# Performance work log

Hardware: AMD Instinct MI355X
Metric: run time of the kernel (lower is better)

Reference implementation:

```python
import jax, jax.numpy as jnp
import numpy as np

DIM = 512
HEADS = 8
DH = 64
INNER = HEADS * DH  # 512
GRID = 32
FH, FW = GRID, GRID // 2 + 1


def _group_norm1(x, g, b, eps=1e-5):
    # GroupNorm(1, C) on NHWC: normalize over (H, W, C) per sample, per-channel affine
    mu = jnp.mean(x, axis=(1, 2, 3), keepdims=True)
    var = jnp.var(x, axis=(1, 2, 3), keepdims=True)
    return (x - mu) * jax.lax.rsqrt(var + eps) * g + b


def setup_inputs() -> dict:
    key = jax.random.key(0)
    ks = jax.random.split(key, 12)
    B, N, C = 8, GRID * GRID + 1, DIM
    s = 0.02
    return {
        "x": jax.random.normal(ks[0], (B, N, C), jnp.float32),
        "Wq": jax.random.normal(ks[1], (C, INNER), jnp.float32) * s,
        "Wk": jax.random.normal(ks[2], (C, INNER), jnp.float32) * s,
        "Wv": jax.random.normal(ks[3], (C, INNER), jnp.float32) * s,
        "dw_w": jax.random.normal(ks[4], (3, 3, 1, C), jnp.float32) * s,   # depthwise, HWIO
        "pw_w": jax.random.normal(ks[5], (C, INNER), jnp.float32) * s,     # 1x1 conv
        "ln_g": jnp.ones((INNER,), jnp.float32),
        "ln_b": jnp.zeros((INNER,), jnp.float32),
        "fr_wr": jnp.ones((FH, FW, C), jnp.float32),    # learnable FFT filter (real)
        "fr_wi": jnp.zeros((FH, FW, C), jnp.float32),   # learnable FFT filter (imag)
        "fr_pw": jax.random.normal(ks[6], (C, INNER), jnp.float32) * s,
        "fr_g": jnp.ones((INNER,), jnp.float32),
        "fr_b": jnp.zeros((INNER,), jnp.float32),
        "g_W1": jax.random.normal(ks[7], (3 * INNER, 3 * INNER // 4), jnp.float32) * s,
        "g_b1": jnp.zeros((3 * INNER // 4,), jnp.float32),
        "g_W2": jax.random.normal(ks[8], (3 * INNER // 4, 3), jnp.float32) * s,
        "g_b2": jnp.zeros((3,), jnp.float32),
        "Wp": jax.random.normal(ks[9], (INNER, DIM), jnp.float32) * s,
        "bp": jnp.zeros((DIM,), jnp.float32),
        "h_feat": GRID,
        "w_feat": GRID,
    }


def reference(x, Wq, Wk, Wv, dw_w, pw_w, ln_g, ln_b, fr_wr, fr_wi, fr_pw, fr_g, fr_b,
              g_W1, g_b1, g_W2, g_b2, Wp, bp, h_feat, w_feat):
    B, N, C = x.shape
    scale = DH ** -0.5
    has_cls = (N == h_feat * w_feat + 1)
    spatial = x[:, 1:] if has_cls else x

    # Branch 1: global self-attention (manual softmax attention)
    q = (x @ Wq).reshape(B, N, HEADS, DH)
    k = (x @ Wk).reshape(B, N, HEADS, DH)
    v = (x @ Wv).reshape(B, N, HEADS, DH)
    attn = jax.nn.softmax(jnp.einsum('bihd,bjhd->bhij', q, k) * scale, axis=-1)
    glob = jnp.einsum('bhij,bjhd->bihd', attn, v).reshape(B, N, INNER)

    # Branch 2: local depthwise conv -> pointwise conv -> GroupNorm(1)
    sp = spatial.reshape(B, h_feat, w_feat, C)  # NHWC
    dw = jax.lax.conv_general_dilated(sp, dw_w, (1, 1), 'SAME',
                                      dimension_numbers=('NHWC', 'HWIO', 'NHWC'),
                                      feature_group_count=C)
    loc = _group_norm1(jnp.einsum('bhwc,co->bhwo', dw, pw_w), ln_g, ln_b)
    loc = loc.reshape(B, h_feat * w_feat, INNER)
    if has_cls:
        loc = jnp.concatenate([loc.mean(axis=1, keepdims=True), loc], axis=1)

    # Branch 3: frequency enhancement (rfft2 -> learnable complex filter -> irfft2)
    xf = jnp.fft.rfft2(sp, axes=(1, 2), norm='ortho')               # (B, FH, FW, C)
    xf = xf * jax.lax.complex(fr_wr, fr_wi)[None]
    xe = jnp.fft.irfft2(xf, s=(h_feat, w_feat), axes=(1, 2), norm='ortho')
    fr = jax.nn.gelu(_group_norm1(jnp.einsum('bhwc,co->bhwo', xe, fr_pw), fr_g, fr_b),
                     approximate=False)
    fr = fr.reshape(B, h_feat * w_feat, INNER)
    if has_cls:
        fr = jnp.concatenate([fr.mean(axis=1, keepdims=True), fr], axis=1)

    # Gate MLP + softmax fusion
    cat = jnp.concatenate([glob, loc, fr], axis=-1)                  # (B, N, 3*INNER)
    gw = jax.nn.softmax(jax.nn.gelu(cat @ g_W1 + g_b1, approximate=False) @ g_W2 + g_b2,
                        axis=-1)                                     # (B, N, 3)
    fused = gw[..., 0:1] * glob + gw[..., 1:2] * loc + gw[..., 2:3] * fr
    return fused @ Wp + bp
```

## Files before the change

kernel.cpp:

```cpp
#include <hip/hip_runtime.h>
#include <math.h>

#define BB 8
#define NT 1025
#define CD 512
#define NH 8
#define DHD 64
#define HW 1024
#define FWD 17
#define MTOK 8200
#define MPAD 8320
#define QKS 1536

typedef __attribute__((ext_vector_type(8))) short short8;
typedef __attribute__((ext_vector_type(4))) float f32x4;
typedef __attribute__((ext_vector_type(16))) float f32x16;
typedef __attribute__((ext_vector_type(4))) unsigned u32x4;

__device__ __forceinline__ float gelu_exact(float x){
  return 0.5f * x * (1.0f + erff(x * 0.70710678118654752f));
}

__device__ __forceinline__ short f2bf(float f){
  unsigned u = __float_as_uint(f);
  unsigned r = (u + 0x7FFFu + ((u >> 16) & 1u)) >> 16;
  return (short)r;
}

__device__ __forceinline__ float bf2f(short s){
  unsigned u = ((unsigned)(unsigned short)s) << 16;
  return __uint_as_float(u);
}

__device__ __forceinline__ unsigned cvt_pk_bf16(float lo, float hi){
  unsigned r;
  asm volatile("v_cvt_pk_bf16_f32 %0, %1, %2" : "=v"(r) : "v"(lo), "v"(hi));
  return r;
}

__device__ __forceinline__ int xcd_logical(int phys, int n){
  int xcd = phys & 7, slot = phys >> 3;
  int q = n >> 3, r = n & 7;
  return xcd*q + (xcd < r ? xcd : r) + slot;
}

__global__ __launch_bounds__(256) void wconv_all(
    const float* __restrict__ Wq, const float* __restrict__ Wk, const float* __restrict__ Wv,
    const float* __restrict__ pw, const float* __restrict__ frpw,
    const float* __restrict__ gW1, const float* __restrict__ Wp,
    short* __restrict__ wqkvt, short* __restrict__ pwt, short* __restrict__ frpwt,
    short* __restrict__ gw1t, short* __restrict__ wpt)
{
  const int t = blockIdx.x;
  const float* W; short* Wt; int K, N, idx; float scale = 1.0f;
  if      (t < 256) { W = Wq;   Wt = wqkvt;            K=512;  N=512; idx=t;       scale=0.125f; }
  else if (t < 512) { W = Wk;   Wt = wqkvt+512*512;    K=512;  N=512; idx=t-256; }
  else if (t < 768) { W = Wv;   Wt = wqkvt+1024*512;   K=512;  N=512; idx=t-512; }
  else if (t < 1024){ W = pw;   Wt = pwt;              K=512;  N=512; idx=t-768; }
  else if (t < 1280){ W = frpw; Wt = frpwt;            K=512;  N=512; idx=t-1024; }
  else if (t < 1856){ W = gW1;  Wt = gw1t;             K=1536; N=384; idx=t-1280; }
  else              { W = Wp;   Wt = wpt;              K=512;  N=512; idx=t-1856; }
  const int ntn = N >> 5;
  const int n0 = (idx % ntn) << 5, k0 = (idx / ntn) << 5;
  __shared__ float tl[32][33];
  const int tx = threadIdx.x & 31, ty = threadIdx.x >> 5;
  #pragma unroll
  for (int i = 0; i < 32; i += 8)
    tl[ty+i][tx] = W[(size_t)(k0+ty+i)*N + n0+tx];
  __syncthreads();
  #pragma unroll
  for (int i = 0; i < 32; i += 8)
    Wt[(size_t)(n0+ty+i)*K + k0+tx] = f2bf(tl[tx][ty+i] * scale);
}

__global__ __launch_bounds__(256) void x2bf(const float* __restrict__ x, short* __restrict__ xb)
{
  size_t i = ((size_t)blockIdx.x*256 + threadIdx.x) * 8;
  if (i >= (size_t)MPAD*CD) return;
  size_t row = i >> 9;
  short8 o;
  if (row < MTOK){
    #pragma unroll
    for (int j = 0; j < 8; j++) o[j] = f2bf(x[i+j]);
  } else {
    #pragma unroll
    for (int j = 0; j < 8; j++) o[j] = 0;
  }
  *(short8*)(xb + i) = o;
}


#define GEMM_DECL                                                          \
  __shared__ short As[2][128*64];                                          \
  __shared__ short Bs[2][64*64];                                           \
  const int tid = threadIdx.x;                                             \
  const int lane = tid & 63, wv = tid >> 6;                                \
  const int lc = lane & 15, lg = lane >> 4;                                \
  short8 ra[4], rb[2];                                                     \
  f32x4 acc[2][4];                                                         \
  _Pragma("unroll")                                                        \
  for (int rt=0;rt<2;rt++)                                                 \
    _Pragma("unroll")                                                      \
    for (int ct=0;ct<4;ct++) acc[rt][ct] = (f32x4){0.f,0.f,0.f,0.f};

#define GEMM_LOADA(Aptr, Kst, k0)                                          \
  _Pragma("unroll")                                                        \
  for (int p = 0; p < 4; p++){                                             \
    int c = tid + p*256; int r = c >> 3, s = c & 7;                        \
    ra[p] = *(const short8*)((Aptr) + (size_t)(row0 + r)*(Kst) + (k0) + s*8); \
  }

#define GEMM_LOADB(Bptr, Kst, k0)                                          \
  _Pragma("unroll")                                                        \
  for (int p = 0; p < 2; p++){                                             \
    int c = tid + p*256; int r = c >> 3, s = c & 7;                        \
    rb[p] = *(const short8*)((Bptr) + (size_t)(col0 + r)*(Kst) + (k0) + s*8); \
  }

#define GEMM_WRITES(buf)                                                   \
  _Pragma("unroll")                                                        \
  for (int p = 0; p < 4; p++){                                             \
    int c = tid + p*256; int r = c >> 3, s = c & 7;                        \
    *(short8*)&As[buf][r*64 + ((s ^ (r & 7))*8)] = ra[p];                  \
  }                                                                        \
  _Pragma("unroll")                                                        \
  for (int p = 0; p < 2; p++){                                             \
    int c = tid + p*256; int r = c >> 3, s = c & 7;                        \
    *(short8*)&Bs[buf][r*64 + ((s ^ (r & 7))*8)] = rb[p];                  \
  }

#define GEMM_COMPUTE(buf)                                                  \
  _Pragma("unroll")                                                        \
  for (int ks = 0; ks < 2; ks++){                                          \
    short8 af[2], bfr[4];                                                  \
    _Pragma("unroll")                                                      \
    for (int rt = 0; rt < 2; rt++){                                        \
      int r = wv*32 + rt*16 + lc;                                          \
      af[rt] = *(const short8*)&As[buf][r*64 + (((ks*4+lg) ^ (r & 7))*8)]; \
    }                                                                      \
    _Pragma("unroll")                                                      \
    for (int ct = 0; ct < 4; ct++){                                        \
      int r = ct*16 + lc;                                                  \
      bfr[ct] = *(const short8*)&Bs[buf][r*64 + (((ks*4+lg) ^ (r & 7))*8)];\
    }                                                                      \
    _Pragma("unroll")                                                      \
    for (int rt = 0; rt < 2; rt++)                                         \
      _Pragma("unroll")                                                    \
      for (int ct = 0; ct < 4; ct++)                                       \
        acc[rt][ct] = __builtin_amdgcn_mfma_f32_16x16x32_bf16(af[rt], bfr[ct], acc[rt][ct], 0,0,0); \
  }

__global__ __launch_bounds__(256) void gemm_bf16(
    const short* __restrict__ A, const short* __restrict__ Bt,
    const float* __restrict__ bias, void* __restrict__ Cm,
    int M, int N, int K, int flags)
{
  const int l = xcd_logical(blockIdx.x, gridDim.x);
  const int nx = N >> 6;
  const int row0 = (l / nx) * 128, col0 = (l % nx) * 64;
  GEMM_DECL;

  const int nk = K >> 6;
  GEMM_LOADA(A, K, 0); GEMM_LOADB(Bt, K, 0);
  GEMM_WRITES(0);
  __syncthreads();
  for (int kt = 0; kt < nk; kt++){
    const int cur = kt & 1;
    if (kt + 1 < nk){ GEMM_LOADA(A, K, (kt+1)*64); GEMM_LOADB(Bt, K, (kt+1)*64); }
    GEMM_COMPUTE(cur);
    if (kt + 1 < nk){
      GEMM_WRITES(cur ^ 1);
      __syncthreads();
    }
  }

  #pragma unroll
  for (int rt = 0; rt < 2; rt++)
    #pragma unroll
    for (int e = 0; e < 4; e++){
      int gr = row0 + wv*32 + rt*16 + lg*4 + e;
      if (gr >= M) continue;
      #pragma unroll
      for (int ct = 0; ct < 4; ct++){
        int gc = col0 + ct*16 + lc;
        float v = acc[rt][ct][e];
        if (flags & 1) v += bias[gc];
        if (flags & 2) v = gelu_exact(v);
        if (flags & 4) ((short*)Cm)[(size_t)gr*N + gc] = f2bf(v);
        else           ((float*)Cm)[(size_t)gr*N + gc] = v;
      }
    }
}

__global__ __launch_bounds__(256) void gemm_pw2(
    const short* __restrict__ A0, const short* __restrict__ B0,
    const short* __restrict__ A1, const short* __restrict__ B1,
    short* __restrict__ C0, short* __restrict__ C1,
    float* __restrict__ totL, float* __restrict__ totF)
{
  const int l = xcd_logical(blockIdx.x, 1024);
  const int bx = l & 7;
  const int by = (l >> 3) & 63;
  const int br = l >> 9;
  const short* A  = br ? A1 : A0;
  const short* Bt = br ? B1 : B0;
  short* Cm       = br ? C1 : C0;
  float* tot      = br ? totF : totL;
  const int N = 512, K = 512;
  const int row0 = by * 128, col0 = bx * 64;
  GEMM_DECL;

  const int nk = 8;
  GEMM_LOADA(A, K, 0); GEMM_LOADB(Bt, K, 0);
  GEMM_WRITES(0);
  __syncthreads();
  for (int kt = 0; kt < nk; kt++){
    const int cur = kt & 1;
    if (kt + 1 < nk){ GEMM_LOADA(A, K, (kt+1)*64); GEMM_LOADB(Bt, K, (kt+1)*64); }
    GEMM_COMPUTE(cur);
    if (kt + 1 < nk){
      GEMM_WRITES(cur ^ 1);
      __syncthreads();
    }
  }

  float s1 = 0.f, s2 = 0.f;
  #pragma unroll
  for (int rt = 0; rt < 2; rt++)
    #pragma unroll
    for (int e = 0; e < 4; e++){
      int gr = row0 + wv*32 + rt*16 + lg*4 + e;
      #pragma unroll
      for (int ct = 0; ct < 4; ct++){
        int gc = col0 + ct*16 + lc;
        float v = acc[rt][ct][e];
        Cm[(size_t)gr*N + gc] = f2bf(v);
        s1 += v; s2 += v*v;
      }
    }
  #pragma unroll
  for (int o = 32; o > 0; o >>= 1){ s1 += __shfl_xor(s1, o); s2 += __shfl_xor(s2, o); }
  if (lane == 0){
    atomicAdd(&tot[(row0>>10)*2],   s1);
    atomicAdd(&tot[(row0>>10)*2+1], s2);
  }
}

__global__ __launch_bounds__(256) void gemm_gate(
    const short* __restrict__ A0, const short* __restrict__ A1, const short* __restrict__ A2,
    const short* __restrict__ Bt, const float* __restrict__ bias, short* __restrict__ Cm,
    int M)
{
  const int N = 384, K = 1536;
  const int l = xcd_logical(blockIdx.x, gridDim.x);
  const int row0 = (l / 6) * 128, col0 = (l % 6) * 64;
  GEMM_DECL;

  const int nk = 24;
  auto loadAg = [&](int kt2){
    int k0 = kt2 * 64;
    const short* Asrc = (k0 < 512) ? A0 : (k0 < 1024 ? A1 : A2);
    const int kb = k0 & 511;
    GEMM_LOADA(Asrc, 512, kb);
  };
  loadAg(0); GEMM_LOADB(Bt, K, 0);
  GEMM_WRITES(0);
  __syncthreads();
  for (int kt = 0; kt < nk; kt++){
    const int cur = kt & 1;
    if (kt + 1 < nk){ loadAg(kt+1); GEMM_LOADB(Bt, K, (kt+1)*64); }
    GEMM_COMPUTE(cur);
    if (kt + 1 < nk){
      GEMM_WRITES(cur ^ 1);
      __syncthreads();
    }
  }

  #pragma unroll
  for (int rt = 0; rt < 2; rt++)
    #pragma unroll
    for (int e = 0; e < 4; e++){
      int gr = row0 + wv*32 + rt*16 + lg*4 + e;
      if (gr >= M) continue;
      #pragma unroll
      for (int ct = 0; ct < 4; ct++){
        int gc = col0 + ct*16 + lc;
        float v = acc[rt][ct][e] + bias[gc];
        Cm[(size_t)gr*N + gc] = f2bf(gelu_exact(v));
      }
    }
}

__global__ __launch_bounds__(256) void attn_mfma32(
    const short* __restrict__ qkv, short* __restrict__ glob)
{
  const int bi = blockIdx.x;
  const int xcd = bi & 7;
  const int jj = bi >> 3;
  const int gq = jj / 9;
  const int qt = jj - gq*9;
  const int g  = xcd + 8*gq;
  const int h  = g & 7, b = g >> 3;

  const int tid = threadIdx.x;
  const int lane = tid & 63, wq = tid >> 6;
  const int q32 = lane & 31;
  const int hi  = lane >> 5;
  const int bN = b * NT;
  const int q0w = qt*128 + wq*32;

  __shared__ short Kl[2][64*64];
  __shared__ short Vl[2][64*64];

  short8 qf[4];
  {
    int qr = q0w + q32; if (qr > 1024) qr = 1024;
    const short* qp = qkv + (size_t)(bN + qr)*QKS + h*DHD + hi*8;
    qf[0] = *(const short8*)(qp);
    qf[1] = *(const short8*)(qp + 16);
    qf[2] = *(const short8*)(qp + 32);
    qf[3] = *(const short8*)(qp + 48);
  }

  f32x16 oA = {0.f,0.f,0.f,0.f,0.f,0.f,0.f,0.f,0.f,0.f,0.f,0.f,0.f,0.f,0.f,0.f};
  f32x16 oB = oA;
  float rs = 0.f;

  const int kc0 = tid;
  const int kc1 = tid + 256;
  const int vkey = tid & 63, vdg = tid >> 6;
  const short* kgbase = qkv + (size_t)bN*QKS + 512 + h*DHD;
  const short* vgbase = qkv + (size_t)bN*QKS + 1024 + h*DHD;

  short8 gk0, gk1, gv0, gv1;
  auto loadT = [&](int kt2){
    gk0 = *(const short8*)(kgbase + (size_t)(kt2*64 + (kc0>>3))*QKS + (kc0&7)*8);
    gk1 = *(const short8*)(kgbase + (size_t)(kt2*64 + (kc1>>3))*QKS + (kc1&7)*8);
    gv0 = *(const short8*)(vgbase + (size_t)(kt2*64 + vkey)*QKS + vdg*16);
    gv1 = *(const short8*)(vgbase + (size_t)(kt2*64 + vkey)*QKS + vdg*16 + 8);
  };
  auto writeT = [&](int buf){
    { int r = kc0>>3, sl = kc0&7;
      *(short8*)&Kl[buf][r*64 + (((sl) ^ (r&7))*8)] = gk0; }
    { int r = kc1>>3, sl = kc1&7;
      *(short8*)&Kl[buf][r*64 + (((sl) ^ (r&7))*8)] = gk1; }
    #pragma unroll
    for (int i2 = 0; i2 < 8; i2++){
      int d0 = vdg*16 + i2, d1 = vdg*16 + 8 + i2;
      Vl[buf][d0*64 + (((vkey>>3) ^ (d0&7))*8) + (vkey&7)] = gv0[i2];
      Vl[buf][d1*64 + (((vkey>>3) ^ (d1&7))*8) + (vkey&7)] = gv1[i2];
    }
  };

  loadT(0);
  writeT(0);
  __syncthreads();

  for (int kt = 0; kt < 17; kt++){
    const int cur = kt & 1;
    if (kt < 16) loadT(kt+1);

    #pragma unroll
    for (int ks = 0; ks < 2; ks++){
      f32x16 s = {0.f,0.f,0.f,0.f,0.f,0.f,0.f,0.f,0.f,0.f,0.f,0.f,0.f,0.f,0.f,0.f};
      const int krow = ks*32 + q32;
      const int kbase = krow*64;
      const int kx = q32 & 7;
      __builtin_amdgcn_s_setprio(1);
      #pragma unroll
      for (int kk = 0; kk < 4; kk++){
        short8 af = *(const short8*)&Kl[cur][kbase + (((2*kk+hi) ^ kx)*8)];
        s = __builtin_amdgcn_mfma_f32_32x32x16_bf16(af, qf[kk], s, 0,0,0);
      }
      __builtin_amdgcn_s_setprio(0);
      float p[16];
      if (kt == 16){
        #pragma unroll
        for (int e = 0; e < 16; e++){
          bool valid = (ks == 0) && (e == 0) && (hi == 0);
          p[e] = valid ? __expf(s[e]) : 0.f;
        }
      } else {
        #pragma unroll
        for (int e = 0; e < 16; e++) p[e] = __expf(s[e]);
      }
      #pragma unroll
      for (int e = 0; e < 16; e++) rs += p[e];
      unsigned pk[4][2];
      #pragma unroll
      for (int g2 = 0; g2 < 4; g2++){
        pk[g2][0] = cvt_pk_bf16(p[4*g2+0], p[4*g2+1]);
        pk[g2][1] = cvt_pk_bf16(p[4*g2+2], p[4*g2+3]);
      }
      #pragma unroll
      for (int kc = 0; kc < 2; kc++){
        unsigned e00 = pk[2*kc][0],   e01 = pk[2*kc][1];
        unsigned e10 = pk[2*kc+1][0], e11 = pk[2*kc+1][1];
        unsigned t00 = (unsigned)__shfl_xor((int)e00, 32);
        unsigned t01 = (unsigned)__shfl_xor((int)e01, 32);
        unsigned t10 = (unsigned)__shfl_xor((int)e10, 32);
        unsigned t11 = (unsigned)__shfl_xor((int)e11, 32);
        u32x4 pu;
        pu[0] = hi ? t10 : e00;
        pu[1] = hi ? t11 : e01;
        pu[2] = hi ? e10 : t00;
        pu[3] = hi ? e11 : t01;
        short8 pa = *(short8*)&pu;
        const int vsl = 4*ks + 2*kc + hi;
        __builtin_amdgcn_s_setprio(1);
        {
          short8 vf0 = *(const short8*)&Vl[cur][(q32)*64      + ((vsl ^ kx)*8)];
          oA = __builtin_amdgcn_mfma_f32_32x32x16_bf16(pa, vf0, oA, 0,0,0);
          short8 vf1 = *(const short8*)&Vl[cur][(32+q32)*64   + ((vsl ^ kx)*8)];
          oB = __builtin_amdgcn_mfma_f32_32x32x16_bf16(pa, vf1, oB, 0,0,0);
        }
        __builtin_amdgcn_s_setprio(0);
      }
    }

    if (kt < 16){
      writeT(cur ^ 1);
      __syncthreads();
    }
  }

  float rs_tot = rs + __shfl_xor(rs, 32);
  #pragma unroll
  for (int e = 0; e < 16; e++){
    int rowr = (e & 3) + 8*(e >> 2) + 4*hi;
    int q = q0w + rowr;
    if (q > 1024) continue;
    float inv = 1.0f / __shfl(rs_tot, rowr);
    size_t base = (size_t)(bN + q)*CD + h*DHD + q32;
    glob[base]      = f2bf(oA[e] * inv);
    glob[base + 32] = f2bf(oB[e] * inv);
  }
}

__global__ __launch_bounds__(512) void dwconv(
    const short* __restrict__ xb, const float* __restrict__ w, short* __restrict__ out)
{
  const int c = threadIdx.x;
  const int xx = blockIdx.x & 31;
  const int yg = (blockIdx.x >> 5) & 7;
  const int b  = blockIdx.x >> 8;
  const int y0 = yg << 2;
  float acc[4] = {0.f,0.f,0.f,0.f};
  #pragma unroll
  for (int dx = -1; dx <= 1; dx++){
    int x2 = xx + dx;
    if (x2 < 0 || x2 > 31) continue;
    float col[6];
    #pragma unroll
    for (int r = 0; r < 6; r++){
      int row = y0 - 1 + r;
      col[r] = (row >= 0 && row < 32)
             ? bf2f(xb[((size_t)(b*NT + 1 + row*32 + x2))*CD + c]) : 0.f;
    }
    float w0 = w[(0*3+dx+1)*CD + c];
    float w1 = w[(1*3+dx+1)*CD + c];
    float w2 = w[(2*3+dx+1)*CD + c];
    #pragma unroll
    for (int o = 0; o < 4; o++)
      acc[o] += col[o]*w0 + col[o+1]*w1 + col[o+2]*w2;
  }
  #pragma unroll
  for (int o = 0; o < 4; o++)
    out[((size_t)(b*HW + (y0+o)*32 + xx))*CD + c] = f2bf(acc[o]);
}

__global__ __launch_bounds__(512) void gn_apply2(
    const short* __restrict__ mmL, const short* __restrict__ mmF,
    const float* __restrict__ totL, const float* __restrict__ totF,
    const float* __restrict__ gL, const float* __restrict__ bL,
    const float* __restrict__ gF, const float* __restrict__ bF,
    short* __restrict__ loc, short* __restrict__ fr,
    float* __restrict__ colsumL, float* __restrict__ colsumF)
{
  const int br = blockIdx.x >> 8;
  const int bi = blockIdx.x & 255;
  const int c = threadIdx.x;
  const int b = bi >> 5;
  const int p0 = (bi & 31) << 5;
  const short* mm = br ? mmF : mmL;
  const float* tot = br ? totF : totL;
  short* out = br ? fr : loc;
  float* colsum = br ? colsumF : colsumL;
  const float inv = 1.0f / ((float)HW * CD);
  const float mu = tot[b*2] * inv;
  const float rstd = rsqrtf(tot[b*2+1]*inv - mu*mu + 1e-5f);
  const float gc = (br ? gF : gL)[c], bc = (br ? bF : bL)[c];
  float s = 0.0f;
  for (int r = 0; r < 32; r++){
    int p = p0 + r;
    float v = bf2f(mm[((size_t)b*HW + p)*CD + c]);
    v = (v - mu) * rstd * gc + bc;
    if (br) v = gelu_exact(v);
    out[((size_t)(b*NT + 1 + p))*CD + c] = f2bf(v);
    s += v;
  }
  atomicAdd(&colsum[b*CD + c], s);
}

__global__ __launch_bounds__(512) void colmean_fin2(
    const float* __restrict__ colsumL, const float* __restrict__ colsumF,
    short* __restrict__ loc, short* __restrict__ fr)
{
  const int c = threadIdx.x;
  const int b = blockIdx.x & 7;
  if (blockIdx.x < 8) loc[((size_t)b*NT)*CD + c] = f2bf(colsumL[b*CD + c] * (1.0f/HW));
  else                fr [((size_t)b*NT)*CD + c] = f2bf(colsumF[b*CD + c] * (1.0f/HW));
}

__global__ __launch_bounds__(512) void fft_f1(
    const float* __restrict__ x, float* __restrict__ Ur, float* __restrict__ Ui)
{
  const int c = threadIdx.x;
  const int xx = blockIdx.x & 31;
  const int b = blockIdx.x >> 5;
  __shared__ float ct[32], st[32];
  if (c < 32){ float ang = 6.283185307179586f * c / 32.0f; ct[c] = cosf(ang); st[c] = sinf(ang); }
  __syncthreads();
  float v[32];
  #pragma unroll
  for (int y = 0; y < 32; y++) v[y] = x[((size_t)(b*NT + 1 + y*32 + xx))*CD + c];
  for (int ky = 0; ky <= 16; ky++){
    float sr = 0.f, si = 0.f;
    #pragma unroll
    for (int y = 0; y < 32; y++){
      int idx = (ky*y) & 31;
      sr += v[y]*ct[idx]; si -= v[y]*st[idx];
    }
    size_t o = ((size_t)((b*17+ky)*32+xx))*CD + c;
    Ur[o] = sr; Ui[o] = si;
  }
}

__global__ __launch_bounds__(256) void fft_f2(
    const float* __restrict__ Ur, const float* __restrict__ Ui,
    const float* __restrict__ wr, const float* __restrict__ wi,
    float* __restrict__ Gr, float* __restrict__ Gi)
{
  const int c = (blockIdx.x & 1)*256 + threadIdx.x;
  const int t = blockIdx.x >> 1;
  const int ky = t % 17, b = t / 17;
  __shared__ float ct[32], st[32];
  if (threadIdx.x < 32){ float ang = 6.283185307179586f * threadIdx.x / 32.0f;
    ct[threadIdx.x] = cosf(ang); st[threadIdx.x] = sinf(ang); }
  __syncthreads();
  float ar[32], ai[32];
  #pragma unroll
  for (int kx = 0; kx < 32; kx++){ ar[kx] = 0.f; ai[kx] = 0.f; }
  #pragma unroll
  for (int xx = 0; xx < 32; xx++){
    size_t o = ((size_t)((b*17+ky)*32+xx))*CD + c;
    float ur = Ur[o], ui = Ui[o];
    #pragma unroll
    for (int kx = 0; kx < 32; kx++){
      int idx = (kx*xx) & 31;
      float cc = ct[idx], ss = st[idx];
      ar[kx] += ur*cc + ui*ss;
      ai[kx] += ui*cc - ur*ss;
    }
  }
  #pragma unroll
  for (int kx = 0; kx < FWD; kx++){
    size_t fo = ((size_t)(ky*FWD+kx))*CD + c;
    float fwr = wr[fo], fwi = wi[fo];
    size_t go = ((size_t)((b*17+kx)*32+ky))*CD + c;
    Gr[go] = ar[kx]*fwr - ai[kx]*fwi;
    Gi[go] = ar[kx]*fwi + ai[kx]*fwr;
  }
  if (ky >= 1 && ky <= 15){
    const int ky2 = 32 - ky;
    #pragma unroll
    for (int kx = 0; kx < FWD; kx++){
      int m = (32 - kx) & 31;
      size_t fo = ((size_t)(ky2*FWD+kx))*CD + c;
      float fwr = wr[fo], fwi = wi[fo];
      size_t go = ((size_t)((b*17+kx)*32+ky2))*CD + c;
      Gr[go] = ar[m]*fwr + ai[m]*fwi;
      Gi[go] = ar[m]*fwi - ai[m]*fwr;
    }
  }
}

__global__ __launch_bounds__(256) void fft_f3(
    const float* __restrict__ Gr, const float* __restrict__ Gi,
    float* __restrict__ Tr, float* __restrict__ Ti)
{
  const int c = (blockIdx.x & 1)*256 + threadIdx.x;
  const int t = blockIdx.x >> 1;
  const int kx = t % 17, b = t / 17;
  __shared__ float ct[32], st[32];
  if (threadIdx.x < 32){ float ang = 6.283185307179586f * threadIdx.x / 32.0f;
    ct[threadIdx.x] = cosf(ang); st[threadIdx.x] = sinf(ang); }
  __syncthreads();
  float tr[32], ti[32];
  #pragma unroll
  for (int y = 0; y < 32; y++){ tr[y] = 0.f; ti[y] = 0.f; }
  #pragma unroll
  for (int ky = 0; ky < 32; ky++){
    size_t go = ((size_t)((b*17+kx)*32+ky))*CD + c;
    float gr = Gr[go], gi = Gi[go];
    #pragma unroll
    for (int y = 0; y < 32; y++){
      int idx = (ky*y) & 31;
      float cc = ct[idx], ss = st[idx];
      tr[y] += gr*cc - gi*ss;
      ti[y] += gr*ss + gi*cc;
    }
  }
  #pragma unroll
  for (int y = 0; y < 32; y++){
    size_t to = ((size_t)((b*32+y)*17+kx))*CD + c;
    Tr[to] = tr[y]*(1.0f/32.0f);
    Ti[to] = ti[y]*(1.0f/32.0f);
  }
}

__global__ __launch_bounds__(512) void fft_f4(
    const float* __restrict__ Tr, const float* __restrict__ Ti, short* __restrict__ xe)
{
  const int c = threadIdx.x;
  const int y = blockIdx.x & 31;
  const int b = blockIdx.x >> 5;
  __shared__ float ct[32], st[32];
  if (c < 32){ float ang = 6.283185307179586f * c / 32.0f; ct[c] = cosf(ang); st[c] = sinf(ang); }
  __syncthreads();
  float tr[FWD], ti[FWD];
  #pragma unroll
  for (int kx = 0; kx < FWD; kx++){
    size_t o = ((size_t)((b*32+y)*17+kx))*CD + c;
    tr[kx] = Tr[o]; ti[kx] = Ti[o];
  }
  for (int x2 = 0; x2 < 32; x2++){
    float acc = tr[0] + ((x2 & 1) ? -tr[16] : tr[16]);
    #pragma unroll
    for (int k2 = 1; k2 < 16; k2++){
      int idx = (k2*x2) & 31;
      acc += 2.0f*(tr[k2]*ct[idx] - ti[k2]*st[idx]);
    }
    xe[((size_t)(b*HW + y*32 + x2))*CD + c] = f2bf(acc*(1.0f/32.0f));
  }
}

__global__ __launch_bounds__(512) void gate_fuse(
    const short* __restrict__ h1, const float* __restrict__ gW2, const float* __restrict__ gb2,
    const short* __restrict__ glob, const short* __restrict__ loc, const short* __restrict__ fr,
    short* __restrict__ fused)
{
  const int token = blockIdx.x;
  const int tid = threadIdx.x;
  const int lane = tid & 63, wv = tid >> 6;
  __shared__ float part[8][3];
  __shared__ float gw[3];
  float p0 = 0.f, p1 = 0.f, p2 = 0.f;
  if (tid < 384){
    float h = bf2f(h1[(size_t)token*384 + tid]);
    p0 = h * gW2[tid*3+0]; p1 = h * gW2[tid*3+1]; p2 = h * gW2[tid*3+2];
  }
  #pragma unroll
  for (int o = 32; o > 0; o >>= 1){
    p0 += __shfl_xor(p0, o); p1 += __shfl_xor(p1, o); p2 += __shfl_xor(p2, o);
  }
  if (lane == 0){ part[wv][0] = p0; part[wv][1] = p1; part[wv][2] = p2; }
  __syncthreads();
  if (tid == 0){
    float l0 = gb2[0], l1 = gb2[1], l2 = gb2[2];
    #pragma unroll
    for (int w = 0; w < 8; w++){ l0 += part[w][0]; l1 += part[w][1]; l2 += part[w][2]; }
    float mx = fmaxf(l0, fmaxf(l1, l2));
    float e0 = expf(l0-mx), e1 = expf(l1-mx), e2 = expf(l2-mx);
    float inv = 1.0f/(e0+e1+e2);
    gw[0] = e0*inv; gw[1] = e1*inv; gw[2] = e2*inv;
  }
  __syncthreads();
  size_t o = (size_t)token*CD + tid;
  fused[o] = f2bf(gw[0]*bf2f(glob[o]) + gw[1]*bf2f(loc[o]) + gw[2]*bf2f(fr[o]));
}

extern "C" void kernel_launch(void* const* d_in, const int* in_sizes, int n_in,
                              void* d_out, int out_size, void* d_ws, size_t ws_size,
                              hipStream_t stream)
{
  const float* x     = (const float*)d_in[0];
  const float* Wq    = (const float*)d_in[1];
  const float* Wk    = (const float*)d_in[2];
  const float* Wv    = (const float*)d_in[3];
  const float* dw_w  = (const float*)d_in[4];
  const float* pw_w  = (const float*)d_in[5];
  const float* ln_g  = (const float*)d_in[6];
  const float* ln_b  = (const float*)d_in[7];
  const float* fr_wr = (const float*)d_in[8];
  const float* fr_wi = (const float*)d_in[9];
  const float* fr_pw = (const float*)d_in[10];
  const float* fr_g  = (const float*)d_in[11];
  const float* fr_b  = (const float*)d_in[12];
  const float* g_W1  = (const float*)d_in[13];
  const float* g_b1  = (const float*)d_in[14];
  const float* g_W2  = (const float*)d_in[15];
  const float* g_b2  = (const float*)d_in[16];
  const float* Wp    = (const float*)d_in[17];
  const float* bp    = (const float*)d_in[18];

  float* ws = (float*)d_ws;
  float* scrA = ws;
  float* scrB = scrA + 8388608;
  float* stats = scrB + 4456448;
  float* totL    = stats;
  float* totF    = stats + 16;
  float* colsumL = stats + 64;
  float* colsumF = stats + 64 + 4096;

  const size_t RPAD = 8448;
  short* glob  = (short*)(stats + 16384);
  short* loc   = glob  + RPAD*CD;
  short* fr    = loc   + RPAD*CD;
  short* actbL = fr    + RPAD*CD;
  short* actbF = actbL + RPAD*CD;
  short* fused = actbL;
  short* qkvb  = actbF + RPAD*CD;
  short* xb    = qkvb + (size_t)MPAD*QKS;
  short* wqkvt = xb + (size_t)MPAD*CD;
  short* pwt   = wqkvt + 1536*512;
  short* frpwt = pwt + 512*512;
  short* gw1t  = frpwt + 512*512;
  short* wpt   = gw1t + 384*1536;
  short* mmL = (short*)scrA;
  short* mmF = mmL + (size_t)8192*CD;

  hipMemsetAsync(stats, 0, (64 + 2*4096)*sizeof(float), stream);
  wconv_all<<<2112, 256, 0, stream>>>(Wq, Wk, Wv, pw_w, fr_pw, g_W1, Wp,
                                      wqkvt, pwt, frpwt, gw1t, wpt);
  x2bf<<<2080, 256, 0, stream>>>(x, xb);

  gemm_bf16<<<1560, 256, 0, stream>>>(xb, wqkvt, nullptr, qkvb, MPAD, 1536, 512, 4);
  attn_mfma32<<<576, 256, 0, stream>>>(qkvb, glob);

  dwconv<<<BB*8*32, 512, 0, stream>>>(xb, dw_w, actbL);
  float* Ur = scrA;            float* Ui = scrA + 2228224;
  float* Gr = scrB;            float* Gi = scrB + 2228224;
  float* Tr = scrA;            float* Ti = scrA + 2228224;
  fft_f1<<<BB*32, 512, 0, stream>>>(x, Ur, Ui);
  fft_f2<<<BB*17*2, 256, 0, stream>>>(Ur, Ui, fr_wr, fr_wi, Gr, Gi);
  fft_f3<<<BB*17*2, 256, 0, stream>>>(Gr, Gi, Tr, Ti);
  fft_f4<<<BB*32, 512, 0, stream>>>(Tr, Ti, actbF);

  gemm_pw2<<<1024, 256, 0, stream>>>(actbL, pwt, actbF, frpwt, mmL, mmF, totL, totF);

  gn_apply2<<<512, 512, 0, stream>>>(mmL, mmF, totL, totF, ln_g, ln_b, fr_g, fr_b,
                                     loc, fr, colsumL, colsumF);
  colmean_fin2<<<16, 512, 0, stream>>>(colsumL, colsumF, loc, fr);

  gemm_gate<<<390, 256, 0, stream>>>(glob, loc, fr, gw1t, g_b1, (short*)scrB, MTOK);
  gate_fuse<<<MTOK, 512, 0, stream>>>((short*)scrB, g_W2, g_b2, glob, loc, fr, fused);
  gemm_bf16<<<520, 256, 0, stream>>>(fused, wpt, bp, d_out, MTOK, 512, 512, 1);
}
```

Measured before the change: 323.9 us.

## Use direct global-to-LDS loads in GEMMs and one-wave-per-token gate fuse

The shared GEMM macros drop the register-staged global loads and LDS writes and use global_load_lds 16-byte async copies straight into swizzled shared memory, with the XOR swizzle moved to the source address. This affects gemm_bf16, the pointwise GEMM and the gate GEMM, freeing registers and VALU/LDS-write work. The gate_fuse kernel now gives each token to one wavefront, with no shared memory or block barriers, and launches 4 tokens per block. The risks are the LDS-DMA ordering relative to the existing barriers and coalescing differences from the new per-wave row mapping.

```diff
diff --git a/kernel.cpp b/kernel.cpp
--- a/kernel.cpp
+++ b/kernel.cpp
@@ -36,6 +36,12 @@
   unsigned r;
   asm volatile("v_cvt_pk_bf16_f32 %0, %1, %2" : "=v"(r) : "v"(lo), "v"(hi));
   return r;
+}
+
+typedef const __attribute__((address_space(1))) unsigned GASu;
+typedef __attribute__((address_space(3))) unsigned LASu;
+__device__ __forceinline__ void gload16(const void* g, void* l){
+  __builtin_amdgcn_global_load_lds((GASu*)g, (LASu*)l, 16, 0, 0);
 }
 
 __device__ __forceinline__ int xcd_logical(int phys, int n){
@@ -96,37 +102,26 @@
   const int tid = threadIdx.x;                                             \
   const int lane = tid & 63, wv = tid >> 6;                                \
   const int lc = lane & 15, lg = lane >> 4;                                \
-  short8 ra[4], rb[2];                                                     \
   f32x4 acc[2][4];                                                         \
   _Pragma("unroll")                                                        \
   for (int rt=0;rt<2;rt++)                                                 \
     _Pragma("unroll")                                                      \
     for (int ct=0;ct<4;ct++) acc[rt][ct] = (f32x4){0.f,0.f,0.f,0.f};
 
-#define GEMM_LOADA(Aptr, Kst, k0)                                          \
+#define GEMM_ISSUE(Aptr, Ka, k0a, Bptr, Kb, k0b, buf)                      \
   _Pragma("unroll")                                                        \
   for (int p = 0; p < 4; p++){                                             \
-    int c = tid + p*256; int r = c >> 3, s = c & 7;                        \
-    ra[p] = *(const short8*)((Aptr) + (size_t)(row0 + r)*(Kst) + (k0) + s*8); \
-  }
-
-#define GEMM_LOADB(Bptr, Kst, k0)                                          \
-  _Pragma("unroll")                                                        \
-  for (int p = 0; p < 2; p++){                                             \
-    int c = tid + p*256; int r = c >> 3, s = c & 7;                        \
-    rb[p] = *(const short8*)((Bptr) + (size_t)(col0 + r)*(Kst) + (k0) + s*8); \
-  }
-
-#define GEMM_WRITES(buf)                                                   \
-  _Pragma("unroll")                                                        \
-  for (int p = 0; p < 4; p++){                                             \
-    int c = tid + p*256; int r = c >> 3, s = c & 7;                        \
-    *(short8*)&As[buf][r*64 + ((s ^ (r & 7))*8)] = ra[p];                  \
+    int r0 = wv*32 + p*8;                                                  \
+    int r = r0 + (lane>>3), s = lane & 7;                                  \
+    gload16((Aptr) + (size_t)(row0 + r)*(Ka) + (k0a) + ((s ^ (r&7))*8),    \
+            &As[buf][r0*64]);                                              \
   }                                                                        \
   _Pragma("unroll")                                                        \
   for (int p = 0; p < 2; p++){                                             \
-    int c = tid + p*256; int r = c >> 3, s = c & 7;                        \
-    *(short8*)&Bs[buf][r*64 + ((s ^ (r & 7))*8)] = rb[p];                  \
+    int r0 = wv*16 + p*8;                                                  \
+    int r = r0 + (lane>>3), s = lane & 7;                                  \
+    gload16((Bptr) + (size_t)(col0 + r)*(Kb) + (k0b) + ((s ^ (r&7))*8),    \
+            &Bs[buf][r0*64]);                                              \
   }
 
 #define GEMM_COMPUTE(buf)                                                  \
@@ -161,17 +156,13 @@
   GEMM_DECL;
 
   const int nk = K >> 6;
-  GEMM_LOADA(A, K, 0); GEMM_LOADB(Bt, K, 0);
-  GEMM_WRITES(0);
+  GEMM_ISSUE(A, K, 0, Bt, K, 0, 0);
   __syncthreads();
   for (int kt = 0; kt < nk; kt++){
     const int cur = kt & 1;
-    if (kt + 1 < nk){ GEMM_LOADA(A, K, (kt+1)*64); GEMM_LOADB(Bt, K, (kt+1)*64); }
+    if (kt + 1 < nk){ GEMM_ISSUE(A, K, (kt+1)*64, Bt, K, (kt+1)*64, cur ^ 1); }
     GEMM_COMPUTE(cur);
-    if (kt + 1 < nk){
-      GEMM_WRITES(cur ^ 1);
-      __syncthreads();
-    }
+    if (kt + 1 < nk) __syncthreads();
   }
 
   #pragma unroll
@@ -211,17 +202,13 @@
   GEMM_DECL;
 
   const int nk = 8;
-  GEMM_LOADA(A, K, 0); GEMM_LOADB(Bt, K, 0);
-  GEMM_WRITES(0);
+  GEMM_ISSUE(A, K, 0, Bt, K, 0, 0);
   __syncthreads();
   for (int kt = 0; kt < nk; kt++){
     const int cur = kt & 1;
-    if (kt + 1 < nk){ GEMM_LOADA(A, K, (kt+1)*64); GEMM_LOADB(Bt, K, (kt+1)*64); }
+    if (kt + 1 < nk){ GEMM_ISSUE(A, K, (kt+1)*64, Bt, K, (kt+1)*64, cur ^ 1); }
     GEMM_COMPUTE(cur);
-    if (kt + 1 < nk){
-      GEMM_WRITES(cur ^ 1);
-      __syncthreads();
-    }
+    if (kt + 1 < nk) __syncthreads();
   }
 
   float s1 = 0.f, s2 = 0.f;
@@ -257,23 +244,21 @@
   GEMM_DECL;
 
   const int nk = 24;
-  auto loadAg = [&](int kt2){
-    int k0 = kt2 * 64;
-    const short* Asrc = (k0 < 512) ? A0 : (k0 < 1024 ? A1 : A2);
-    const int kb = k0 & 511;
-    GEMM_LOADA(Asrc, 512, kb);
-  };
-  loadAg(0); GEMM_LOADB(Bt, K, 0);
-  GEMM_WRITES(0);
+  {
+    const short* Asrc = A0;
+    GEMM_ISSUE(Asrc, 512, 0, Bt, K, 0, 0);
+  }
   __syncthreads();
   for (int kt = 0; kt < nk; kt++){
     const int cur = kt & 1;
-    if (kt + 1 < nk){ loadAg(kt+1); GEMM_LOADB(Bt, K, (kt+1)*64); }
+    if (kt + 1 < nk){
+      int k0 = (kt+1) * 64;
+      const short* Asrc = (k0 < 512) ? A0 : (k0 < 1024 ? A1 : A2);
+      const int kb = k0 & 511;
+      GEMM_ISSUE(Asrc, 512, kb, Bt, K, k0, cur ^ 1);
+    }
     GEMM_COMPUTE(cur);
-    if (kt + 1 < nk){
-      GEMM_WRITES(cur ^ 1);
-      __syncthreads();
-    }
+    if (kt + 1 < nk) __syncthreads();
   }
 
   #pragma unroll
@@ -645,39 +630,35 @@
   }
 }
 
-__global__ __launch_bounds__(512) void gate_fuse(
+__global__ __launch_bounds__(256) void gate_fuse(
     const short* __restrict__ h1, const float* __restrict__ gW2, const float* __restrict__ gb2,
     const short* __restrict__ glob, const short* __restrict__ loc, const short* __restrict__ fr,
     short* __restrict__ fused)
 {
-  const int token = blockIdx.x;
-  const int tid = threadIdx.x;
-  const int lane = tid & 63, wv = tid >> 6;
-  __shared__ float part[8][3];
-  __shared__ float gw[3];
+  const int token = blockIdx.x*4 + (threadIdx.x >> 6);
+  const int lane = threadIdx.x & 63;
+  if (token >= MTOK) return;
   float p0 = 0.f, p1 = 0.f, p2 = 0.f;
-  if (tid < 384){
-    float h = bf2f(h1[(size_t)token*384 + tid]);
-    p0 = h * gW2[tid*3+0]; p1 = h * gW2[tid*3+1]; p2 = h * gW2[tid*3+2];
+  #pragma unroll
+  for (int i = 0; i < 6; i++){
+    int idx = lane + i*64;
+    float h = bf2f(h1[(size_t)token*384 + idx]);
+    p0 += h * gW2[idx*3+0]; p1 += h * gW2[idx*3+1]; p2 += h * gW2[idx*3+2];
   }
   #pragma unroll
   for (int o = 32; o > 0; o >>= 1){
     p0 += __shfl_xor(p0, o); p1 += __shfl_xor(p1, o); p2 += __shfl_xor(p2, o);
   }
-  if (lane == 0){ part[wv][0] = p0; part[wv][1] = p1; part[wv][2] = p2; }
-  __syncthreads();
-  if (tid == 0){
-    float l0 = gb2[0], l1 = gb2[1], l2 = gb2[2];
-    #pragma unroll
-    for (int w = 0; w < 8; w++){ l0 += part[w][0]; l1 += part[w][1]; l2 += part[w][2]; }
-    float mx = fmaxf(l0, fmaxf(l1, l2));
-    float e0 = expf(l0-mx), e1 = expf(l1-mx), e2 = expf(l2-mx);
-    float inv = 1.0f/(e0+e1+e2);
-    gw[0] = e0*inv; gw[1] = e1*inv; gw[2] = e2*inv;
-  }
-  __syncthreads();
-  size_t o = (size_t)token*CD + tid;
-  fused[o] = f2bf(gw[0]*bf2f(glob[o]) + gw[1]*bf2f(loc[o]) + gw[2]*bf2f(fr[o]));
+  p0 += gb2[0]; p1 += gb2[1]; p2 += gb2[2];
+  float mx = fmaxf(p0, fmaxf(p1, p2));
+  float e0 = __expf(p0-mx), e1 = __expf(p1-mx), e2 = __expf(p2-mx);
+  float inv = 1.0f/(e0+e1+e2);
+  float g0 = e0*inv, g1 = e1*inv, g2 = e2*inv;
+  #pragma unroll
+  for (int i = 0; i < 8; i++){
+    size_t o2 = (size_t)token*CD + lane + i*64;
+    fused[o2] = f2bf(g0*bf2f(glob[o2]) + g1*bf2f(loc[o2]) + g2*bf2f(fr[o2]));
+  }
 }
 
 extern "C" void kernel_launch(void* const* d_in, const int* in_sizes, int n_in,
@@ -754,6 +735,6 @@
   colmean_fin2<<<16, 512, 0, stream>>>(colsumL, colsumF, loc, fr);
 
   gemm_gate<<<390, 256, 0, stream>>>(glob, loc, fr, gw1t, g_b1, (short*)scrB, MTOK);
-  gate_fuse<<<MTOK, 512, 0, stream>>>((short*)scrB, g_W2, g_b2, glob, loc, fr, fused);
+  gate_fuse<<<2050, 256, 0, stream>>>((short*)scrB, g_W2, g_b2, glob, loc, fr, fused);
   gemm_bf16<<<520, 256, 0, stream>>>(fused, wpt, bp, d_out, MTOK, 512, 512, 1);
 }
```

After: 324.7 us. About the same (+0.3%).
